# Performance work log

Measured on AMD Instinct MI355X. Metric: run time of the kernel, lower is better.

## Reference

```python
import jax, jax.numpy as jnp
import numpy as np

TAU = 0.1
EPS = 1e-8  # torch CosineSimilarity eps


def setup_inputs() -> dict:
    key = jax.random.key(0)
    k1, k2, k3 = jax.random.split(key, 3)
    B, D = 4096, 128
    z_i = jax.random.normal(k1, (B, D), dtype=jnp.float32)
    z_j = jax.random.normal(k2, (B, D), dtype=jnp.float32)
    y = jax.random.randint(k3, (B,), 0, 2)
    return {"z_i": z_i, "z_j": z_j, "y": y}


def reference(z_i, z_j, y):
    # p: (N, D) with N = 2B
    p = jnp.concatenate([z_i, z_j], axis=0)
    # cosine similarity via row-normalization + matmul (same math as the
    # broadcasted torch CosineSimilarity, without the O(N^2*D) intermediate)
    norm = jnp.maximum(jnp.linalg.norm(p, axis=1, keepdims=True), EPS)
    pn = p / norm
    sim = jnp.einsum('id,jd->ij', pn, pn) / TAU  # (N, N)

    N = sim.shape[0]
    y2 = jnp.concatenate([y, y], axis=0)
    eye = jnp.eye(N, dtype=sim.dtype)
    pos_mask = (y2[:, None] == y2[None, :]).astype(sim.dtype) * (1.0 - eye)
    logit_mask = 1.0 - eye

    # denominator excludes the diagonal (self-similarity)
    exp_logits = jnp.exp(sim) * logit_mask
    log_prob = sim - jnp.log(jnp.sum(exp_logits, axis=1, keepdims=True))
    mean_log_prob_pos = jnp.sum(pos_mask * log_prob, axis=1) / jnp.sum(pos_mask, axis=1)
    loss = -jnp.sum(mean_log_prob_pos)
    return loss
```

## Files before the change

### kernel.cpp

```cpp
#include <hip/hip_runtime.h>
#include <math.h>

#define BSZ 4096
#define NROW 8192
#define DIM 128
#define LOG2E10 14.426950408889634f

typedef __attribute__((ext_vector_type(8))) short bf16x8;
typedef __attribute__((ext_vector_type(4))) float f32x4;

#define PNH_F     (NROW * DIM / 2)
#define G_OFF     PNH_F
#define CNT_OFF   (G_OFF + 256)
#define SPART_OFF (G_OFF + 512)
#define PART_OFF  (SPART_OFF + 16 * NROW)

__device__ __forceinline__ float bf2f(unsigned short h) {
    return __uint_as_float(((unsigned)h) << 16);
}
__device__ __forceinline__ unsigned short f2bf(float f) {
    unsigned u = __float_as_uint(f);
    return (unsigned short)((u + 0x7FFF + ((u >> 16) & 1)) >> 16);
}

__global__ void k_norm(const float* __restrict__ zi, const float* __restrict__ zj,
                       unsigned short* __restrict__ pnh) {
    int tid  = threadIdx.x;
    int wave = tid >> 6, lane = tid & 63;
    int row  = blockIdx.x * 4 + wave;
    const float* src = (row < BSZ) ? (zi + (size_t)row * DIM)
                                   : (zj + (size_t)(row - BSZ) * DIM);
    float2 v = ((const float2*)src)[lane];
    float ss = v.x * v.x + v.y * v.y;
    #pragma unroll
    for (int m = 32; m; m >>= 1) ss += __shfl_xor(ss, m, 64);
    float inv = 1.0f / fmaxf(sqrtf(ss), 1e-8f);
    unsigned short h0 = f2bf(v.x * inv), h1 = f2bf(v.y * inv);
    ((unsigned*)(pnh + (size_t)row * DIM))[lane] = (unsigned)h0 | ((unsigned)h1 << 16);
}

__global__ void k_colsum(const unsigned short* __restrict__ pnh, const int* __restrict__ y,
                         float* __restrict__ g, float* __restrict__ cnt) {
    __shared__ float r0[256], r1[256];
    int tid = threadIdx.x;
    if (blockIdx.x < DIM) {
        int d = blockIdx.x;
        float s0 = 0.f, s1 = 0.f;
        for (int r = tid; r < NROW; r += 256) {
            int lab = y[r & (BSZ - 1)];
            float v = bf2f(pnh[(size_t)r * DIM + d]);
            if (lab) s1 += v; else s0 += v;
        }
        r0[tid] = s0; r1[tid] = s1;
        __syncthreads();
        for (int s = 128; s; s >>= 1) {
            if (tid < s) { r0[tid] += r0[tid + s]; r1[tid] += r1[tid + s]; }
            __syncthreads();
        }
        if (tid == 0) { g[d] = r0[0]; g[DIM + d] = r1[0]; }
    } else {
        float c = 0.f;
        for (int r = tid; r < BSZ; r += 256) c += (float)y[r];
        r0[tid] = c;
        __syncthreads();
        for (int s = 128; s; s >>= 1) {
            if (tid < s) r0[tid] += r0[tid + s];
            __syncthreads();
        }
        if (tid == 0) { cnt[1] = 2.0f * r0[0]; cnt[0] = (float)NROW - 2.0f * r0[0]; }
    }
}

__global__ __launch_bounds__(256, 2)
void k_expsum(const unsigned short* __restrict__ pnh, float* __restrict__ spart) {
    __shared__ short bt[2][128 * 128];
    int tid  = threadIdx.x;
    int lane = tid & 63;
    int wave = tid >> 6;
    int wr = wave & 1, wc = wave >> 1;
    int l15 = lane & 15, q = lane >> 4;
    int rowBase = blockIdx.x * 128;
    int chunk   = blockIdx.y;

    bf16x8 a[4][4];
    const unsigned short* abase = pnh + (size_t)(rowBase + wr * 64 + l15) * DIM + q * 8;
    #pragma unroll
    for (int r = 0; r < 4; ++r)
        #pragma unroll
        for (int ks = 0; ks < 4; ++ks)
            a[r][ks] = *(const bf16x8*)(abase + (size_t)r * 16 * DIM + ks * 32);

    float rs[4][4];
    #pragma unroll
    for (int r = 0; r < 4; ++r)
        #pragma unroll
        for (int e = 0; e < 4; ++e) rs[r][e] = 0.f;

    auto stage = [&](int s, int b) {
        const float4* src = (const float4*)(pnh + (size_t)(chunk * 1024 + s * 128) * DIM);
        #pragma unroll
        for (int i = 0; i < 8; ++i) {
            int idx = tid + 256 * i;
            int row = idx >> 4, j = idx & 15;
            float4 v = src[idx];
            *(float4*)(&bt[b][row * 128 + ((j ^ (row & 15)) << 3)]) = v;
        }
    };

    stage(0, 0);
    __syncthreads();

    for (int s = 0; s < 8; ++s) {
        int cur = s & 1;
        if (s < 7) stage(s + 1, cur ^ 1);

        f32x4 acc[4][4];
        #pragma unroll
        for (int r = 0; r < 4; ++r)
            #pragma unroll
            for (int c = 0; c < 4; ++c) acc[r][c] = (f32x4){0.f, 0.f, 0.f, 0.f};

        const short* buf = bt[cur];
        #pragma unroll
        for (int ks = 0; ks < 4; ++ks)
            #pragma unroll
            for (int c = 0; c < 4; ++c) {
                int bcol = wc * 64 + c * 16 + l15;
                bf16x8 bfrag = *(const bf16x8*)(buf + bcol * 128 + (((ks * 4 + q) ^ l15) << 3));
                #pragma unroll
                for (int r = 0; r < 4; ++r)
                    acc[r][c] = __builtin_amdgcn_mfma_f32_16x16x32_bf16(a[r][ks], bfrag, acc[r][c], 0, 0, 0);
            }

        int colBase = chunk * 1024 + s * 128;
        bool diagBlk = (rowBase == colBase);
        #pragma unroll
        for (int r = 0; r < 4; ++r)
            #pragma unroll
            for (int c = 0; c < 4; ++c) {
                int cl = wc * 64 + c * 16 + l15;
                #pragma unroll
                for (int e = 0; e < 4; ++e) {
                    int rl = wr * 64 + r * 16 + q * 4 + e;
                    float ex = exp2f(acc[r][c][e] * LOG2E10);
                    if (diagBlk && rl == cl) ex = 0.f;
                    rs[r][e] += ex;
                }
            }
        __syncthreads();
    }

    #pragma unroll
    for (int r = 0; r < 4; ++r)
        #pragma unroll
        for (int e = 0; e < 4; ++e) {
            float v = rs[r][e];
            v += __shfl_xor(v, 1, 16);
            v += __shfl_xor(v, 2, 16);
            v += __shfl_xor(v, 4, 16);
            v += __shfl_xor(v, 8, 16);
            if (l15 == 0)
                spart[(size_t)(chunk * 2 + wc) * NROW + rowBase + wr * 64 + r * 16 + q * 4 + e] = v;
        }
}

__global__ void k_finalize(const unsigned short* __restrict__ pnh, const float* __restrict__ spart,
                           const float* __restrict__ g, const float* __restrict__ cnt,
                           const int* __restrict__ y, float* __restrict__ partial) {
    __shared__ float red[256];
    int row = blockIdx.x * 256 + threadIdx.x;
    float S = 0.f;
    #pragma unroll
    for (int ch = 0; ch < 16; ++ch) S += spart[(size_t)ch * NROW + row];
    int lab = y[row & (BSZ - 1)];
    float C = cnt[lab] - 1.0f;
    const unsigned short* pr = pnh + (size_t)row * DIM;
    const float* gl = g + lab * DIM;
    float dg = 0.f, dself = 0.f;
    #pragma unroll
    for (int d = 0; d < DIM; d += 8) {
        uint4 u = *(const uint4*)(pr + d);
        float p0 = __uint_as_float(u.x << 16), p1 = __uint_as_float(u.x & 0xFFFF0000u);
        float p2 = __uint_as_float(u.y << 16), p3 = __uint_as_float(u.y & 0xFFFF0000u);
        float p4 = __uint_as_float(u.z << 16), p5 = __uint_as_float(u.z & 0xFFFF0000u);
        float p6 = __uint_as_float(u.w << 16), p7 = __uint_as_float(u.w & 0xFFFF0000u);
        float4 g0 = *(const float4*)(gl + d);
        float4 g1 = *(const float4*)(gl + d + 4);
        dg    += p0 * g0.x + p1 * g0.y + p2 * g0.z + p3 * g0.w
               + p4 * g1.x + p5 * g1.y + p6 * g1.z + p7 * g1.w;
        dself += p0 * p0 + p1 * p1 + p2 * p2 + p3 * p3
               + p4 * p4 + p5 * p5 + p6 * p6 + p7 * p7;
    }
    float P = (dg - dself) * 10.0f;
    float contrib = logf(S) - P / C;
    red[threadIdx.x] = contrib;
    __syncthreads();
    for (int s = 128; s; s >>= 1) {
        if (threadIdx.x < s) red[threadIdx.x] += red[threadIdx.x + s];
        __syncthreads();
    }
    if (threadIdx.x == 0) partial[blockIdx.x] = red[0];
}

__global__ void k_sum(const float* __restrict__ partial, float* __restrict__ out) {
    float v = (threadIdx.x < 32) ? partial[threadIdx.x] : 0.f;
    #pragma unroll
    for (int m = 32; m; m >>= 1) v += __shfl_xor(v, m, 64);
    if (threadIdx.x == 0) out[0] = v;
}

extern "C" void kernel_launch(void* const* d_in, const int* in_sizes, int n_in,
                              void* d_out, int out_size, void* d_ws, size_t ws_size,
                              hipStream_t stream) {
    const float* zi = (const float*)d_in[0];
    const float* zj = (const float*)d_in[1];
    const int*   y  = (const int*)d_in[2];
    float* out = (float*)d_out;
    float* ws  = (float*)d_ws;

    unsigned short* pnh = (unsigned short*)ws;
    float* g       = ws + G_OFF;
    float* cnt     = ws + CNT_OFF;
    float* spart   = ws + SPART_OFF;
    float* partial = ws + PART_OFF;

    k_norm<<<NROW / 4, 256, 0, stream>>>(zi, zj, pnh);
    k_colsum<<<DIM + 1, 256, 0, stream>>>(pnh, y, g, cnt);
    k_expsum<<<dim3(NROW / 128, 8), 256, 0, stream>>>(pnh, spart);
    k_finalize<<<NROW / 256, 256, 0, stream>>>(pnh, spart, g, cnt, y, partial);
    k_sum<<<1, 64, 0, stream>>>(partial, out);
}
```

Before: 115.8 us.

## Restructure all kernels for coalesced column sums, smaller expsum tiles, wave-per-row finalize

The column-sum kernel now reads contiguous row segments across 128 blocks and combines the per-block results with atomicAdd into g, which k_norm zeroes first, replacing strided per-dimension column reads. The exp-sum kernel switches to 32-row waves against 64-column tiles, doubling the grid to 16 column chunks, and raises the launch-bounds occupancy hint from 2 to 4. It also adds a fast path that skips the diagonal mask for tiles that cannot touch the diagonal. Finalize now uses one wave per row with shuffle reductions instead of one thread looping over a whole row, and k_sum reduces 2048 partials. The smaller tiles lower B-operand reuse per wave, and the atomics make the float summation order nondeterministic.

```diff
diff --git a/kernel.cpp b/kernel.cpp
--- a/kernel.cpp
+++ b/kernel.cpp
@@ -15,17 +15,15 @@
 #define SPART_OFF (G_OFF + 512)
 #define PART_OFF  (SPART_OFF + 16 * NROW)
 
-__device__ __forceinline__ float bf2f(unsigned short h) {
-    return __uint_as_float(((unsigned)h) << 16);
-}
 __device__ __forceinline__ unsigned short f2bf(float f) {
     unsigned u = __float_as_uint(f);
     return (unsigned short)((u + 0x7FFF + ((u >> 16) & 1)) >> 16);
 }
 
 __global__ void k_norm(const float* __restrict__ zi, const float* __restrict__ zj,
-                       unsigned short* __restrict__ pnh) {
+                       unsigned short* __restrict__ pnh, float* __restrict__ g) {
     int tid  = threadIdx.x;
+    if (blockIdx.x == 0) g[tid] = 0.f;
     int wave = tid >> 6, lane = tid & 63;
     int row  = blockIdx.x * 4 + wave;
     const float* src = (row < BSZ) ? (zi + (size_t)row * DIM)
@@ -41,24 +39,32 @@
 
 __global__ void k_colsum(const unsigned short* __restrict__ pnh, const int* __restrict__ y,
                          float* __restrict__ g, float* __restrict__ cnt) {
-    __shared__ float r0[256], r1[256];
+    __shared__ float red[4][4][64];
     int tid = threadIdx.x;
-    if (blockIdx.x < DIM) {
-        int d = blockIdx.x;
-        float s0 = 0.f, s1 = 0.f;
-        for (int r = tid; r < NROW; r += 256) {
-            int lab = y[r & (BSZ - 1)];
-            float v = bf2f(pnh[(size_t)r * DIM + d]);
-            if (lab) s1 += v; else s0 += v;
-        }
-        r0[tid] = s0; r1[tid] = s1;
-        __syncthreads();
-        for (int s = 128; s; s >>= 1) {
-            if (tid < s) { r0[tid] += r0[tid + s]; r1[tid] += r1[tid + s]; }
-            __syncthreads();
-        }
-        if (tid == 0) { g[d] = r0[0]; g[DIM + d] = r1[0]; }
+    if (blockIdx.x < 128) {
+        int d2 = tid & 63;
+        int rg = tid >> 6;
+        int row0 = blockIdx.x * 64 + rg * 16;
+        float s0a = 0.f, s0b = 0.f, s1a = 0.f, s1b = 0.f;
+        #pragma unroll 4
+        for (int i = 0; i < 16; ++i) {
+            int r = row0 + i;
+            unsigned u = ((const unsigned*)(pnh + (size_t)r * DIM))[d2];
+            float va = __uint_as_float(u << 16);
+            float vb = __uint_as_float(u & 0xFFFF0000u);
+            if (y[r & (BSZ - 1)]) { s1a += va; s1b += vb; }
+            else                  { s0a += va; s0b += vb; }
+        }
+        red[rg][0][d2] = s0a; red[rg][1][d2] = s0b;
+        red[rg][2][d2] = s1a; red[rg][3][d2] = s1b;
+        __syncthreads();
+        int lab = tid >> 7, d = tid & 127;
+        int which = lab * 2 + (d & 1), dd2 = d >> 1;
+        float s = red[0][which][dd2] + red[1][which][dd2]
+                + red[2][which][dd2] + red[3][which][dd2];
+        atomicAdd(&g[lab * DIM + d], s);
     } else {
+        __shared__ float r0[256];
         float c = 0.f;
         for (int r = tid; r < BSZ; r += 256) c += (float)y[r];
         r0[tid] = c;
@@ -71,35 +77,35 @@
     }
 }
 
-__global__ __launch_bounds__(256, 2)
+__global__ __launch_bounds__(256, 4)
 void k_expsum(const unsigned short* __restrict__ pnh, float* __restrict__ spart) {
-    __shared__ short bt[2][128 * 128];
+    __shared__ short bt[2][64 * 128];
     int tid  = threadIdx.x;
     int lane = tid & 63;
-    int wave = tid >> 6;
-    int wr = wave & 1, wc = wave >> 1;
+    int w    = tid >> 6;
     int l15 = lane & 15, q = lane >> 4;
     int rowBase = blockIdx.x * 128;
     int chunk   = blockIdx.y;
-
-    bf16x8 a[4][4];
-    const unsigned short* abase = pnh + (size_t)(rowBase + wr * 64 + l15) * DIM + q * 8;
-    #pragma unroll
-    for (int r = 0; r < 4; ++r)
+    int rwb     = rowBase + w * 32;
+
+    bf16x8 a[2][4];
+    const unsigned short* abase = pnh + (size_t)(rwb + l15) * DIM + q * 8;
+    #pragma unroll
+    for (int rf = 0; rf < 2; ++rf)
         #pragma unroll
         for (int ks = 0; ks < 4; ++ks)
-            a[r][ks] = *(const bf16x8*)(abase + (size_t)r * 16 * DIM + ks * 32);
-
-    float rs[4][4];
-    #pragma unroll
-    for (int r = 0; r < 4; ++r)
-        #pragma unroll
-        for (int e = 0; e < 4; ++e) rs[r][e] = 0.f;
+            a[rf][ks] = *(const bf16x8*)(abase + (size_t)rf * 16 * DIM + ks * 32);
+
+    float rs[2][4];
+    #pragma unroll
+    for (int rf = 0; rf < 2; ++rf)
+        #pragma unroll
+        for (int e = 0; e < 4; ++e) rs[rf][e] = 0.f;
 
     auto stage = [&](int s, int b) {
-        const float4* src = (const float4*)(pnh + (size_t)(chunk * 1024 + s * 128) * DIM);
-        #pragma unroll
-        for (int i = 0; i < 8; ++i) {
+        const float4* src = (const float4*)(pnh + (size_t)(chunk * 512 + s * 64) * DIM);
+        #pragma unroll
+        for (int i = 0; i < 4; ++i) {
             int idx = tid + 256 * i;
             int row = idx >> 4, j = idx & 15;
             float4 v = src[idx];
@@ -114,99 +120,105 @@
         int cur = s & 1;
         if (s < 7) stage(s + 1, cur ^ 1);
 
-        f32x4 acc[4][4];
-        #pragma unroll
-        for (int r = 0; r < 4; ++r)
-            #pragma unroll
-            for (int c = 0; c < 4; ++c) acc[r][c] = (f32x4){0.f, 0.f, 0.f, 0.f};
+        f32x4 acc[2][4];
+        #pragma unroll
+        for (int rf = 0; rf < 2; ++rf)
+            #pragma unroll
+            for (int c = 0; c < 4; ++c) acc[rf][c] = (f32x4){0.f, 0.f, 0.f, 0.f};
 
         const short* buf = bt[cur];
         #pragma unroll
         for (int ks = 0; ks < 4; ++ks)
             #pragma unroll
             for (int c = 0; c < 4; ++c) {
-                int bcol = wc * 64 + c * 16 + l15;
-                bf16x8 bfrag = *(const bf16x8*)(buf + bcol * 128 + (((ks * 4 + q) ^ l15) << 3));
+                bf16x8 bfrag = *(const bf16x8*)(buf + (c * 16 + l15) * 128 + (((ks * 4 + q) ^ l15) << 3));
+                acc[0][c] = __builtin_amdgcn_mfma_f32_16x16x32_bf16(a[0][ks], bfrag, acc[0][c], 0, 0, 0);
+                acc[1][c] = __builtin_amdgcn_mfma_f32_16x16x32_bf16(a[1][ks], bfrag, acc[1][c], 0, 0, 0);
+            }
+
+        int cb = chunk * 512 + s * 64;
+        bool dia = (cb < rwb + 32) && (rwb < cb + 64);
+        if (dia) {
+            #pragma unroll
+            for (int rf = 0; rf < 2; ++rf)
                 #pragma unroll
-                for (int r = 0; r < 4; ++r)
-                    acc[r][c] = __builtin_amdgcn_mfma_f32_16x16x32_bf16(a[r][ks], bfrag, acc[r][c], 0, 0, 0);
-            }
-
-        int colBase = chunk * 1024 + s * 128;
-        bool diagBlk = (rowBase == colBase);
-        #pragma unroll
-        for (int r = 0; r < 4; ++r)
-            #pragma unroll
-            for (int c = 0; c < 4; ++c) {
-                int cl = wc * 64 + c * 16 + l15;
+                for (int c = 0; c < 4; ++c) {
+                    int col = cb + c * 16 + l15;
+                    #pragma unroll
+                    for (int e = 0; e < 4; ++e) {
+                        int row = rwb + rf * 16 + q * 4 + e;
+                        float ex = exp2f(acc[rf][c][e] * LOG2E10);
+                        if (row == col) ex = 0.f;
+                        rs[rf][e] += ex;
+                    }
+                }
+        } else {
+            #pragma unroll
+            for (int rf = 0; rf < 2; ++rf)
                 #pragma unroll
-                for (int e = 0; e < 4; ++e) {
-                    int rl = wr * 64 + r * 16 + q * 4 + e;
-                    float ex = exp2f(acc[r][c][e] * LOG2E10);
-                    if (diagBlk && rl == cl) ex = 0.f;
-                    rs[r][e] += ex;
-                }
-            }
-        __syncthreads();
-    }
-
-    #pragma unroll
-    for (int r = 0; r < 4; ++r)
+                for (int c = 0; c < 4; ++c)
+                    #pragma unroll
+                    for (int e = 0; e < 4; ++e)
+                        rs[rf][e] += exp2f(acc[rf][c][e] * LOG2E10);
+        }
+        __syncthreads();
+    }
+
+    #pragma unroll
+    for (int rf = 0; rf < 2; ++rf)
         #pragma unroll
         for (int e = 0; e < 4; ++e) {
-            float v = rs[r][e];
+            float v = rs[rf][e];
             v += __shfl_xor(v, 1, 16);
             v += __shfl_xor(v, 2, 16);
             v += __shfl_xor(v, 4, 16);
             v += __shfl_xor(v, 8, 16);
             if (l15 == 0)
-                spart[(size_t)(chunk * 2 + wc) * NROW + rowBase + wr * 64 + r * 16 + q * 4 + e] = v;
+                spart[(size_t)chunk * NROW + rwb + rf * 16 + q * 4 + e] = v;
         }
 }
 
 __global__ void k_finalize(const unsigned short* __restrict__ pnh, const float* __restrict__ spart,
                            const float* __restrict__ g, const float* __restrict__ cnt,
                            const int* __restrict__ y, float* __restrict__ partial) {
+    __shared__ float red[4];
+    int tid = threadIdx.x, wv = tid >> 6, lane = tid & 63;
+    int row = blockIdx.x * 4 + wv;
+    int lab = y[row & (BSZ - 1)];
+    unsigned u = ((const unsigned*)(pnh + (size_t)row * DIM))[lane];
+    float p0 = __uint_as_float(u << 16);
+    float p1 = __uint_as_float(u & 0xFFFF0000u);
+    float2 gv = ((const float2*)(g + lab * DIM))[lane];
+    float dg = p0 * gv.x + p1 * gv.y;
+    float ds = p0 * p0 + p1 * p1;
+    float sp = (lane < 16) ? spart[(size_t)lane * NROW + row] : 0.f;
+    #pragma unroll
+    for (int m = 32; m; m >>= 1) {
+        dg += __shfl_xor(dg, m, 64);
+        ds += __shfl_xor(ds, m, 64);
+        sp += __shfl_xor(sp, m, 64);
+    }
+    if (lane == 0) {
+        float C = cnt[lab] - 1.0f;
+        float P = (dg - ds) * 10.0f;
+        red[wv] = logf(sp) - P / C;
+    }
+    __syncthreads();
+    if (tid == 0) partial[blockIdx.x] = red[0] + red[1] + red[2] + red[3];
+}
+
+__global__ void k_sum(const float* __restrict__ partial, float* __restrict__ out) {
     __shared__ float red[256];
-    int row = blockIdx.x * 256 + threadIdx.x;
-    float S = 0.f;
-    #pragma unroll
-    for (int ch = 0; ch < 16; ++ch) S += spart[(size_t)ch * NROW + row];
-    int lab = y[row & (BSZ - 1)];
-    float C = cnt[lab] - 1.0f;
-    const unsigned short* pr = pnh + (size_t)row * DIM;
-    const float* gl = g + lab * DIM;
-    float dg = 0.f, dself = 0.f;
-    #pragma unroll
-    for (int d = 0; d < DIM; d += 8) {
-        uint4 u = *(const uint4*)(pr + d);
-        float p0 = __uint_as_float(u.x << 16), p1 = __uint_as_float(u.x & 0xFFFF0000u);
-        float p2 = __uint_as_float(u.y << 16), p3 = __uint_as_float(u.y & 0xFFFF0000u);
-        float p4 = __uint_as_float(u.z << 16), p5 = __uint_as_float(u.z & 0xFFFF0000u);
-        float p6 = __uint_as_float(u.w << 16), p7 = __uint_as_float(u.w & 0xFFFF0000u);
-        float4 g0 = *(const float4*)(gl + d);
-        float4 g1 = *(const float4*)(gl + d + 4);
-        dg    += p0 * g0.x + p1 * g0.y + p2 * g0.z + p3 * g0.w
-               + p4 * g1.x + p5 * g1.y + p6 * g1.z + p7 * g1.w;
-        dself += p0 * p0 + p1 * p1 + p2 * p2 + p3 * p3
-               + p4 * p4 + p5 * p5 + p6 * p6 + p7 * p7;
-    }
-    float P = (dg - dself) * 10.0f;
-    float contrib = logf(S) - P / C;
-    red[threadIdx.x] = contrib;
+    float v = 0.f;
+    #pragma unroll
+    for (int i = 0; i < 8; ++i) v += partial[threadIdx.x + 256 * i];
+    red[threadIdx.x] = v;
     __syncthreads();
     for (int s = 128; s; s >>= 1) {
         if (threadIdx.x < s) red[threadIdx.x] += red[threadIdx.x + s];
         __syncthreads();
     }
-    if (threadIdx.x == 0) partial[blockIdx.x] = red[0];
-}
-
-__global__ void k_sum(const float* __restrict__ partial, float* __restrict__ out) {
-    float v = (threadIdx.x < 32) ? partial[threadIdx.x] : 0.f;
-    #pragma unroll
-    for (int m = 32; m; m >>= 1) v += __shfl_xor(v, m, 64);
-    if (threadIdx.x == 0) out[0] = v;
+    if (threadIdx.x == 0) out[0] = red[0];
 }
 
 extern "C" void kernel_launch(void* const* d_in, const int* in_sizes, int n_in,
@@ -224,9 +236,9 @@
     float* spart   = ws + SPART_OFF;
     float* partial = ws + PART_OFF;
 
-    k_norm<<<NROW / 4, 256, 0, stream>>>(zi, zj, pnh);
-    k_colsum<<<DIM + 1, 256, 0, stream>>>(pnh, y, g, cnt);
-    k_expsum<<<dim3(NROW / 128, 8), 256, 0, stream>>>(pnh, spart);
-    k_finalize<<<NROW / 256, 256, 0, stream>>>(pnh, spart, g, cnt, y, partial);
-    k_sum<<<1, 64, 0, stream>>>(partial, out);
-}
+    k_norm<<<NROW / 4, 256, 0, stream>>>(zi, zj, pnh, g);
+    k_colsum<<<129, 256, 0, stream>>>(pnh, y, g, cnt);
+    k_expsum<<<dim3(NROW / 128, 16), 256, 0, stream>>>(pnh, spart);
+    k_finalize<<<NROW / 4, 256, 0, stream>>>(pnh, spart, g, cnt, y, partial);
+    k_sum<<<1, 256, 0, stream>>>(partial, out);
+}
```

After: 105.1 us. -9.2%, faster.
